# Performance work log

Measured on AMD Instinct MI355X. Metric: run time of the kernel, lower is better.

The kernel has to match this reference:

```python
import jax, jax.numpy as jnp
import numpy as np

L, B, N, C, H = 8, 8, 512, 1024, 16
D = C // H
TP = (2.0 * D) ** 0.5  # temperature_coeff * head_dim, sqrt


def _ln(x):
    # LayerNorm(eps=1e-6, no affine)
    m = jnp.mean(x, axis=-1, keepdims=True)
    v = jnp.var(x, axis=-1, keepdims=True)
    return (x - m) * jax.lax.rsqrt(v + 1e-6)


def _modulate(x, shift, scale):
    return x * (1 + scale) + shift


def setup_inputs() -> dict:
    key = jax.random.key(0)
    ks = jax.random.split(key, 18)
    s = 0.02
    return {
        "x": jax.random.normal(ks[0], (B, N, C), dtype=jnp.float32),
        "time": jax.random.uniform(ks[1], (B, 1), dtype=jnp.float32) * 100.0,
        "label": jax.random.normal(ks[2], (B, 2), dtype=jnp.float32),
        "x_mask": jax.random.randint(ks[3], (B, N, 1), 0, 2).astype(jnp.float32),
        # ValueLabelEmbed: Linear(2 -> C)
        "Wl": jax.random.normal(ks[4], (C, 2), dtype=jnp.float32) * s,
        "bl": jnp.zeros((C,), dtype=jnp.float32),
        # per-layer stacked weights (leading dim L)
        "Wq": jax.random.normal(ks[5], (L, C, C), dtype=jnp.float32) * s,
        "Wk": jax.random.normal(ks[6], (L, C, C), dtype=jnp.float32) * s,
        "Wv": jax.random.normal(ks[7], (L, C, C), dtype=jnp.float32) * s,
        "W1": jax.random.normal(ks[8], (L, 4 * C, C), dtype=jnp.float32) * s,
        "b1": jnp.zeros((L, 4 * C), dtype=jnp.float32),
        "W2": jax.random.normal(ks[9], (L, C, 4 * C), dtype=jnp.float32) * s,
        "b2": jnp.zeros((L, C), dtype=jnp.float32),
        "Wm": jax.random.normal(ks[10], (L, 6 * C, C), dtype=jnp.float32) * s,
        "bm": jnp.zeros((L, 6 * C), dtype=jnp.float32),
        # FinalLayer
        "Wf": jax.random.normal(ks[11], (C, C), dtype=jnp.float32) * s,
        "bf": jnp.zeros((C,), dtype=jnp.float32),
        "Wmf": jax.random.normal(ks[12], (2 * C, C), dtype=jnp.float32) * s,
        "bmf": jnp.zeros((2 * C,), dtype=jnp.float32),
    }


def reference(x, time, label, x_mask, Wl, bl, Wq, Wk, Wv, W1, b1, W2, b2, Wm, bm, Wf, bf, Wmf, bmf):
    # ValueLabelEmbed: (B,2) -> (B,1,C)
    lemb = (label @ Wl.T + bl)[:, None, :]
    # TimeEmbedding: interleaved sin/cos of time / 10000^(2i/d)
    base = jnp.power(10000.0, 2.0 * jnp.arange(C, dtype=jnp.float32) / C)
    te = time / base  # (B, C)
    even = (jnp.arange(C) % 2) == 0
    te = jnp.where(even, jnp.sin(te), jnp.cos(te))
    c = lemb + te[:, None, :]  # (B,1,C)

    # self-attention mask: True where exactly one of the pair is valid
    xm = x_mask[:, :, 0]  # (B,N)
    mask = ((xm[:, :, None] + xm[:, None, :]) == 1.0)[:, None, :, :]  # (B,1,N,N)

    def block(xc, p):
        wq, wk, wv, w1, bb1, w2, bb2, wm, bbm = p
        m6 = jax.nn.selu(c) @ wm.T + bbm  # (B,1,6C)
        sm, sc, gm, sf, cf, gf = jnp.split(m6, 6, axis=-1)
        h = _modulate(_ln(xc), sm, sc) * x_mask
        q = (h @ wq.T).reshape(B, N, H, D)
        k = (h @ wk.T).reshape(B, N, H, D)
        v = (h @ wv.T).reshape(B, N, H, D)
        scores = jnp.einsum('bqhd,bkhd->bhqk', q, k) / TP
        scores = jnp.where(mask, -jnp.inf, scores)
        alpha = jax.nn.softmax(scores, axis=-1)
        att = jnp.einsum('bhqk,bkhd->bqhd', alpha, v).reshape(B, N, C)
        xc = xc + gm * att
        h2 = _modulate(_ln(xc), sf, cf)
        ffn = jax.nn.selu(h2 @ w1.T + bb1) @ w2.T + bb2
        xc = (xc + gf * ffn) * x_mask
        return xc, None

    x, _ = jax.lax.scan(block, x, (Wq, Wk, Wv, W1, b1, W2, b2, Wm, bm))

    # FinalLayer
    m2 = jax.nn.selu(c) @ Wmf.T + bmf
    shift, scale = jnp.split(m2, 2, axis=-1)
    out = (_modulate(_ln(x), shift, scale) @ Wf.T + bf) * x_mask
    return out
```

## Files before the change

### kernel.cpp

```cpp
#include <hip/hip_runtime.h>
#include <hip/hip_bf16.h>
#include <cstddef>

#define DEVI __device__ __forceinline__

typedef __attribute__((ext_vector_type(4))) float f4v;
typedef __attribute__((ext_vector_type(16))) float f16v;
typedef __attribute__((ext_vector_type(8))) short s8v;
typedef __attribute__((ext_vector_type(4))) short s4v;

using bf16 = __hip_bfloat16;

constexpr float SELU_A = 1.6732632423543772f;
constexpr float SELU_S = 1.0507009873554805f;
constexpr float TPINV  = 0.08838834764831845f;

DEVI float bfbits(short s) { return __uint_as_float(((unsigned)(unsigned short)s) << 16); }
DEVI unsigned short f2bu(float f) {
  bf16 h = __float2bfloat16(f);
  return __builtin_bit_cast(unsigned short, h);
}
DEVI float seluf(float x) { return x > 0.f ? SELU_S * x : SELU_S * SELU_A * (__expf(x) - 1.f); }

DEVI void gl16(const void* g, void* l) {
  __builtin_amdgcn_global_load_lds((__attribute__((address_space(1))) void*)g,
                                   (__attribute__((address_space(3))) void*)l, 16, 0, 0);
}

DEVI void conv8(const float* __restrict__ src, bf16* __restrict__ dst) {
  f4v a = *(const f4v*)src;
  f4v b = *(const f4v*)(src + 4);
  s8v o;
  #pragma unroll
  for (int j = 0; j < 4; j++) { o[j] = (short)f2bu(a[j]); o[4 + j] = (short)f2bu(b[j]); }
  *(s8v*)dst = o;
}

__global__ void k_compact(const float* __restrict__ xm, int* __restrict__ idx,
                          int* __restrict__ pos, int* __restrict__ cnt,
                          int* __restrict__ start, int* __restrict__ t2b)
{
  int t = threadIdx.x;
  int b = t >> 6, lane = t & 63;
  __shared__ int scnt[8];
  int base = b * 512 + lane * 8;
  int mb[8]; int lc = 0;
  #pragma unroll
  for (int i = 0; i < 8; i++) { mb[i] = (xm[base + i] != 0.f) ? 1 : 0; lc += mb[i]; }
  int s = lc;
  #pragma unroll
  for (int o = 1; o < 64; o <<= 1) { int tt = __shfl_up(s, o); if (lane >= o) s += tt; }
  int run = s - lc;
  #pragma unroll
  for (int i = 0; i < 8; i++) {
    int n = lane * 8 + i;
    if (mb[i]) { idx[b * 512 + run] = n; pos[b * 512 + n] = run; run++; }
    else pos[b * 512 + n] = -1;
  }
  if (lane == 63) scnt[b] = s;
  __syncthreads();
  if (t == 0) {
    int st = 0, tile = 0;
    for (int bb = 0; bb < 8; bb++) {
      cnt[bb] = scnt[bb];
      start[bb] = st;
      int nt = (scnt[bb] + 127) >> 7;
      for (int k = 0; k < nt; k++) t2b[tile++] = bb;
      st += nt * 128;
    }
    start[8] = st;
    for (; tile < 32; tile++) t2b[tile] = 0;
  }
}

__global__ __launch_bounds__(256) void k_gather(const float* __restrict__ xin,
    const int* __restrict__ idx, const int* __restrict__ cnt,
    const int* __restrict__ start, const int* __restrict__ t2b,
    float* __restrict__ xc)
{
  int row = blockIdx.x, t = threadIdx.x;
  if (row >= start[8]) return;
  int tb = t2b[row >> 7], slot = row - start[tb];
  f4v v = {0.f, 0.f, 0.f, 0.f};
  if (slot < cnt[tb])
    v = *(const f4v*)&xin[((size_t)tb * 512 + idx[tb * 512 + slot]) * 1024 + t * 4];
  *(f4v*)&xc[(size_t)row * 1024 + t * 4] = v;
}

__global__ __launch_bounds__(256) void k_scatter(const float* __restrict__ ffin,
    const int* __restrict__ pos, const int* __restrict__ start, float* __restrict__ out)
{
  int row = blockIdx.x, t = threadIdx.x, b = row >> 9;
  int p = pos[row];
  f4v v = {0.f, 0.f, 0.f, 0.f};
  if (p >= 0) v = *(const f4v*)&ffin[(size_t)(start[b] + p) * 1024 + t * 4];
  *(f4v*)&out[(size_t)row * 1024 + t * 4] = v;
}

__global__ __launch_bounds__(256) void k_convall(
    const float* __restrict__ wq, const float* __restrict__ wk, const float* __restrict__ wv,
    const float* __restrict__ w1, const float* __restrict__ w2,
    bf16* __restrict__ wqkvb, bf16* __restrict__ w1b, bf16* __restrict__ w2b)
{
  int i = blockIdx.x * 256 + threadIdx.x;
  if (i < 393216) {
    int o = i * 8;
    int row = o >> 10, col = o & 1023;
    int sel = row >> 10, sr = row & 1023;
    conv8((sel == 0 ? wq : sel == 1 ? wk : wv) + (size_t)sr * 1024 + col, wqkvb + o);
  } else if (i < 917504) {
    size_t o = (size_t)(i - 393216) * 8;
    conv8(w1 + o, w1b + o);
  } else if (i < 1441792) {
    size_t o = (size_t)(i - 917504) * 8;
    conv8(w2 + o, w2b + o);
  }
}

__global__ void k_cond(const float* __restrict__ tim, const float* __restrict__ lab,
                       const float* __restrict__ Wl, const float* __restrict__ bl,
                       float* __restrict__ cs)
{
  int b = blockIdx.x, t = threadIdx.x;
  float l0 = lab[b * 2 + 0], l1 = lab[b * 2 + 1], tv = tim[b];
  #pragma unroll
  for (int i = 0; i < 4; i++) {
    int j = t + 256 * i;
    float e = powf(10000.f, (2.f * (float)j) * (1.f / 1024.f));
    float arg = tv / e;
    float te = ((j & 1) == 0) ? sinf(arg) : cosf(arg);
    float c = l0 * Wl[j * 2 + 0] + l1 * Wl[j * 2 + 1] + bl[j] + te;
    cs[b * 1024 + j] = seluf(c);
  }
}

__global__ __launch_bounds__(256) void k_small(
    const float* __restrict__ cs, const float* __restrict__ W, const float* __restrict__ bias,
    float* __restrict__ out, int O, int mode)
{
  __shared__ float cls[8192];
  int t = threadIdx.x;
  #pragma unroll
  for (int i = 0; i < 8; i++)
    *(f4v*)&cls[i * 1024 + t * 4] = *(const f4v*)&cs[i * 1024 + t * 4];
  __syncthreads();
  int w = t >> 6, l = t & 63;
  int o = blockIdx.x * 4 + w;
  if (o >= O) return;
  float acc[8] = {0.f, 0.f, 0.f, 0.f, 0.f, 0.f, 0.f, 0.f};
  const float* Wr = W + (size_t)o * 1024;
  for (int i = 0; i < 16; i++) {
    int k = i * 64 + l;
    float wv = Wr[k];
    #pragma unroll
    for (int b = 0; b < 8; b++) acc[b] += wv * cls[b * 1024 + k];
  }
  #pragma unroll
  for (int b = 0; b < 8; b++) {
    #pragma unroll
    for (int off = 32; off; off >>= 1) acc[b] += __shfl_xor(acc[b], off);
  }
  float bv = bias[o];
  #pragma unroll
  for (int b = 0; b < 8; b++) {
    if (l == b) {
      float val = acc[b] + bv;
      size_t dst;
      if (mode == 0) { int ll = o / 6144, ft = o - ll * 6144; dst = ((size_t)ll * 8 + b) * 6144 + ft; }
      else dst = (size_t)b * 2048 + o;
      out[dst] = val;
    }
  }
}

__global__ __launch_bounds__(256) void k_lnmod(
    const float* __restrict__ x, const float* __restrict__ shiftB, const float* __restrict__ scaleB,
    int bstride, const int* __restrict__ cnt, const int* __restrict__ start,
    const int* __restrict__ t2b, bf16* __restrict__ out)
{
  int row = blockIdx.x, t = threadIdx.x;
  if (row >= start[8]) return;
  int tb = t2b[row >> 7], slot = row - start[tb];
  if (slot >= cnt[tb]) {
    s4v z = {0, 0, 0, 0};
    *(s4v*)&out[(size_t)row * 1024 + t * 4] = z;
    return;
  }
  const float* xr = x + (size_t)row * 1024;
  f4v v = *(const f4v*)&xr[t * 4];
  float s = v[0] + v[1] + v[2] + v[3];
  float ss = v[0]*v[0] + v[1]*v[1] + v[2]*v[2] + v[3]*v[3];
  #pragma unroll
  for (int off = 32; off; off >>= 1) { s += __shfl_xor(s, off); ss += __shfl_xor(ss, off); }
  __shared__ float rs[4], rss[4];
  int w = t >> 6;
  if ((t & 63) == 0) { rs[w] = s; rss[w] = ss; }
  __syncthreads();
  s = rs[0] + rs[1] + rs[2] + rs[3];
  ss = rss[0] + rss[1] + rss[2] + rss[3];
  float mean = s * (1.f / 1024.f);
  float var = ss * (1.f / 1024.f) - mean * mean;
  float rstd = rsqrtf(var + 1e-6f);
  f4v sh = *(const f4v*)&shiftB[(size_t)tb * bstride + t * 4];
  f4v sc = *(const f4v*)&scaleB[(size_t)tb * bstride + t * 4];
  s4v o;
  #pragma unroll
  for (int i = 0; i < 4; i++)
    o[i] = (short)f2bu((v[i] - mean) * rstd * (1.f + sc[i]) + sh[i]);
  *(s4v*)&out[(size_t)row * 1024 + t * 4] = o;
}

__global__ __launch_bounds__(256) void k_resid(
    float* __restrict__ x, const bf16* __restrict__ att, const float* __restrict__ m6b,
    const int* __restrict__ cnt, const int* __restrict__ start,
    const int* __restrict__ t2b, bf16* __restrict__ h2)
{
  int row = blockIdx.x, t = threadIdx.x;
  if (row >= start[8]) return;
  int tb = t2b[row >> 7], slot = row - start[tb];
  if (slot >= cnt[tb]) {
    s4v z = {0, 0, 0, 0};
    *(s4v*)&h2[(size_t)row * 1024 + t * 4] = z;
    return;
  }
  float* xr = x + (size_t)row * 1024;
  const float* gm = m6b + (size_t)tb * 6144 + 2048;
  const float* sf = m6b + (size_t)tb * 6144 + 3072;
  const float* cf = m6b + (size_t)tb * 6144 + 4096;
  f4v xv = *(const f4v*)&xr[t * 4];
  s4v av = *(const s4v*)&att[((size_t)tb * 512 + slot) * 1024 + t * 4];
  f4v gv = *(const f4v*)&gm[t * 4];
  f4v vv;
  #pragma unroll
  for (int i = 0; i < 4; i++) vv[i] = xv[i] + gv[i] * bfbits(av[i]);
  *(f4v*)&xr[t * 4] = vv;
  float s = vv[0] + vv[1] + vv[2] + vv[3];
  float ss = vv[0]*vv[0] + vv[1]*vv[1] + vv[2]*vv[2] + vv[3]*vv[3];
  #pragma unroll
  for (int off = 32; off; off >>= 1) { s += __shfl_xor(s, off); ss += __shfl_xor(ss, off); }
  __shared__ float rs[4], rss[4];
  int w = t >> 6;
  if ((t & 63) == 0) { rs[w] = s; rss[w] = ss; }
  __syncthreads();
  s = rs[0] + rs[1] + rs[2] + rs[3];
  ss = rss[0] + rss[1] + rss[2] + rss[3];
  float mean = s * (1.f / 1024.f);
  float var = ss * (1.f / 1024.f) - mean * mean;
  float rstd = rsqrtf(var + 1e-6f);
  f4v sfv = *(const f4v*)&sf[t * 4];
  f4v cfv = *(const f4v*)&cf[t * 4];
  s4v o;
  #pragma unroll
  for (int i = 0; i < 4; i++)
    o[i] = (short)f2bu((vv[i] - mean) * rstd * (1.f + cfv[i]) + sfv[i]);
  *(s4v*)&h2[(size_t)row * 1024 + t * 4] = o;
}

__global__ __launch_bounds__(256) void k_attn(
    const bf16* __restrict__ q, const bf16* __restrict__ k, const bf16* __restrict__ vt,
    const int* __restrict__ cnt, bf16* __restrict__ att,
    const float* __restrict__ nwq, const float* __restrict__ nwk, const float* __restrict__ nwv,
    const float* __restrict__ nw1, const float* __restrict__ nw2,
    bf16* __restrict__ dqkv, bf16* __restrict__ dw1, bf16* __restrict__ dw2, int mode)
{
  if (blockIdx.x >= 4) {
    int cid = (blockIdx.x - 4) * 128 + blockIdx.y;
    int i0 = cid * 256 + threadIdx.x;
    #pragma unroll
    for (int half = 0; half < 2; half++) {
      int j = i0 * 2 + half;
      if (mode == 1) {
        if (j < 131072) conv8(nwq + (size_t)j * 8, dqkv + (size_t)j * 8);
      } else {
        if (j < 393216) {
          int o = j * 8;
          int row = o >> 10, col = o & 1023;
          int sel = row >> 10, sr = row & 1023;
          conv8((sel == 0 ? nwq : sel == 1 ? nwk : nwv) + (size_t)sr * 1024 + col, dqkv + o);
        } else if (j < 917504) {
          size_t o = (size_t)(j - 393216) * 8;
          conv8(nw1 + o, dw1 + o);
        } else {
          size_t o = (size_t)(j - 917504) * 8;
          conv8(nw2 + o, dw2 + o);
        }
      }
    }
    return;
  }

  int bh = blockIdx.y, b = bh >> 4, hh = bh & 15;
  int cntb = cnt[b];
  if ((int)blockIdx.x * 128 >= cntb) return;
  int t = threadIdx.x, w = t >> 6, lane = t & 63;
  int fr = lane & 15, g = lane >> 4;
  int qw = blockIdx.x * 128 + w * 32;
  const size_t ho = (size_t)bh * (512 * 64);

  __shared__ bf16 Pb[4][32][72];

  s8v qf[2][2];
  #pragma unroll
  for (int mf = 0; mf < 2; mf++)
    #pragma unroll
    for (int kk = 0; kk < 2; kk++)
      qf[mf][kk] = *(const s8v*)(q + ho + (size_t)(qw + mf * 16 + fr) * 64 + kk * 32 + g * 8);

  float mrow[2][4], lsum[2][4];
  f4v oacc[2][4];
  const f4v vzero = {0.f, 0.f, 0.f, 0.f};
  #pragma unroll
  for (int mf = 0; mf < 2; mf++)
    #pragma unroll
    for (int r = 0; r < 4; r++) { mrow[mf][r] = -3.0e38f; lsum[mf][r] = 0.f; }
  #pragma unroll
  for (int mf = 0; mf < 2; mf++)
    #pragma unroll
    for (int nd = 0; nd < 4; nd++) oacc[mf][nd] = vzero;

  int nkt = (cntb + 63) >> 6;
  for (int kt = 0; kt < nkt; kt++) {
    int kb0 = kt * 64;
    f4v sacc[2][4];
    #pragma unroll
    for (int mf = 0; mf < 2; mf++)
      #pragma unroll
      for (int nf = 0; nf < 4; nf++) sacc[mf][nf] = vzero;
    #pragma unroll
    for (int kk = 0; kk < 2; kk++) {
      s8v kf[4];
      #pragma unroll
      for (int nf = 0; nf < 4; nf++)
        kf[nf] = *(const s8v*)(k + ho + (size_t)(kb0 + nf * 16 + fr) * 64 + kk * 32 + g * 8);
      #pragma unroll
      for (int mf = 0; mf < 2; mf++)
        #pragma unroll
        for (int nf = 0; nf < 4; nf++)
          sacc[mf][nf] = __builtin_amdgcn_mfma_f32_16x16x32_bf16(qf[mf][kk], kf[nf], sacc[mf][nf], 0, 0, 0);
    }
    #pragma unroll
    for (int mf = 0; mf < 2; mf++) {
      #pragma unroll
      for (int r = 0; r < 4; r++) {
        float mx = -3.0e38f;
        #pragma unroll
        for (int nf = 0; nf < 4; nf++) {
          float s = sacc[mf][nf][r] * TPINV;
          if (kb0 + nf * 16 + fr >= cntb) s = -1.0e30f;
          sacc[mf][nf][r] = s;
          mx = fmaxf(mx, s);
        }
        mx = fmaxf(mx, __shfl_xor(mx, 1));
        mx = fmaxf(mx, __shfl_xor(mx, 2));
        mx = fmaxf(mx, __shfl_xor(mx, 4));
        mx = fmaxf(mx, __shfl_xor(mx, 8));
        float mnew = fmaxf(mrow[mf][r], mx);
        float corr = __expf(mrow[mf][r] - mnew);
        mrow[mf][r] = mnew;
        float ps = 0.f;
        #pragma unroll
        for (int nf = 0; nf < 4; nf++) {
          float p = __expf(sacc[mf][nf][r] - mnew);
          ps += p;
          Pb[w][mf * 16 + g * 4 + r][nf * 16 + fr] = __float2bfloat16(p);
        }
        lsum[mf][r] = lsum[mf][r] * corr + ps;
        #pragma unroll
        for (int nd = 0; nd < 4; nd++) oacc[mf][nd][r] *= corr;
      }
    }
    #pragma unroll
    for (int kk = 0; kk < 2; kk++) {
      s8v pf[2], vf[4];
      #pragma unroll
      for (int mf = 0; mf < 2; mf++)
        pf[mf] = *(const s8v*)&Pb[w][mf * 16 + fr][kk * 32 + g * 8];
      #pragma unroll
      for (int nd = 0; nd < 4; nd++)
        vf[nd] = *(const s8v*)(vt + ho + (size_t)(nd * 16 + fr) * 512 + kb0 + kk * 32 + g * 8);
      #pragma unroll
      for (int mf = 0; mf < 2; mf++)
        #pragma unroll
        for (int nd = 0; nd < 4; nd++)
          oacc[mf][nd] = __builtin_amdgcn_mfma_f32_16x16x32_bf16(pf[mf], vf[nd], oacc[mf][nd], 0, 0, 0);
    }
  }
  float inv[2][4];
  #pragma unroll
  for (int mf = 0; mf < 2; mf++)
    #pragma unroll
    for (int r = 0; r < 4; r++) {
      float ls = lsum[mf][r];
      ls += __shfl_xor(ls, 1);
      ls += __shfl_xor(ls, 2);
      ls += __shfl_xor(ls, 4);
      ls += __shfl_xor(ls, 8);
      inv[mf][r] = 1.f / ls;
    }
  #pragma unroll
  for (int mf = 0; mf < 2; mf++)
    #pragma unroll
    for (int nd = 0; nd < 4; nd++)
      #pragma unroll
      for (int r = 0; r < 4; r++) {
        int row = qw + mf * 16 + g * 4 + r;
        att[(size_t)(b * 512 + row) * 1024 + hh * 64 + nd * 16 + fr] =
            __float2bfloat16(oacc[mf][nd][r] * inv[mf][r]);
      }
}

template <int EPI, int BN>
__global__ __launch_bounds__(256) void k_gemm(
    const bf16* __restrict__ A, const bf16* __restrict__ W,
    const float* __restrict__ bias, int Kst, int kLen, int Ncols,
    const int* __restrict__ cnt, const int* __restrict__ start, const int* __restrict__ t2b,
    bf16* __restrict__ outb, float* __restrict__ outf)
{
  constexpr int NFR = BN / 64;
  constexpr int NW  = BN / 32;
  __shared__ bf16 As[128][64];
  __shared__ bf16 Ws[BN][64];
  int t = threadIdx.x, lane = t & 63, w = t >> 6;
  int wr = w >> 1, wc = w & 1;
  int m0 = blockIdx.y * 128, n0 = blockIdx.x * BN;
  if (m0 >= start[8]) return;
  int kOff = blockIdx.z * kLen;
  int r32 = lane & 31, hi = lane >> 5;

  const bf16* Abase = A + (size_t)m0 * Kst + kOff;
  const bf16* Wbase = W + (size_t)n0 * Kst + kOff;

  f16v acc[2][NFR];
  #pragma unroll
  for (int i = 0; i < 2; i++)
    #pragma unroll
    for (int j = 0; j < NFR; j++)
      #pragma unroll
      for (int e = 0; e < 16; e++) acc[i][j][e] = 0.f;

  int nkt = kLen >> 6;
  for (int kt = 0; kt < nkt; kt++) {
    int k0 = kt << 6;
    __syncthreads();
    #pragma unroll
    for (int i = 0; i < 4; i++) {
      int Z = w * 4096 + i * 1024 + lane * 16;
      int row = Z >> 7, slot = (Z >> 4) & 7;
      int ss = slot ^ (row & 7);
      gl16(Abase + (size_t)row * Kst + k0 + ss * 8, (char*)As + Z);
    }
    #pragma unroll
    for (int i = 0; i < NW; i++) {
      int Z = w * (NW * 1024) + i * 1024 + lane * 16;
      int row = Z >> 7, slot = (Z >> 4) & 7;
      int ss = slot ^ (row & 7);
      gl16(Wbase + (size_t)row * Kst + k0 + ss * 8, (char*)Ws + Z);
    }
    __syncthreads();
    #pragma unroll
    for (int kk = 0; kk < 4; kk++) {
      s8v af[2], bfr[NFR];
      #pragma unroll
      for (int mf = 0; mf < 2; mf++) {
        int row = wr * 64 + mf * 32 + r32;
        int sl = (kk * 2 + hi) ^ (row & 7);
        af[mf] = *(const s8v*)((const char*)As + row * 128 + sl * 16);
      }
      #pragma unroll
      for (int nf = 0; nf < NFR; nf++) {
        int row = wc * (BN / 2) + nf * 32 + r32;
        int sl = (kk * 2 + hi) ^ (row & 7);
        bfr[nf] = *(const s8v*)((const char*)Ws + row * 128 + sl * 16);
      }
      #pragma unroll
      for (int mf = 0; mf < 2; mf++)
        #pragma unroll
        for (int nf = 0; nf < NFR; nf++)
          acc[mf][nf] = __builtin_amdgcn_mfma_f32_32x32x16_bf16(af[mf], bfr[nf], acc[mf][nf], 0, 0, 0);
    }
  }

  int tb = t2b[m0 >> 7];
  int sb = start[tb];
  #pragma unroll
  for (int mf = 0; mf < 2; mf++) {
    #pragma unroll
    for (int nf = 0; nf < NFR; nf++) {
      int col = n0 + wc * (BN / 2) + nf * 32 + r32;
      #pragma unroll
      for (int qd = 0; qd < 4; qd++) {
        int row0 = m0 + wr * 64 + mf * 32 + qd * 8 + hi * 4;
        if (EPI == 0) {
          int sel = col >> 10, cl = col & 1023;
          int nn = row0 - sb;
          int h2 = cl >> 6, dd = cl & 63;
          if (sel == 2) {
            s4v o4;
            #pragma unroll
            for (int r = 0; r < 4; r++) o4[r] = (short)f2bu(acc[mf][nf][qd * 4 + r]);
            *(s4v*)&outb[(size_t)2 * 4194304 + (((size_t)tb * 16 + h2) * 64 + dd) * 512 + nn] = o4;
          } else {
            #pragma unroll
            for (int r = 0; r < 4; r++)
              outb[(size_t)sel * 4194304 + (((size_t)tb * 16 + h2) * 512 + (nn + r)) * 64 + dd] =
                  __float2bfloat16(acc[mf][nf][qd * 4 + r]);
          }
        } else {
          #pragma unroll
          for (int r = 0; r < 4; r++) {
            int row = row0 + r;
            float val = acc[mf][nf][qd * 4 + r];
            if (EPI == 1) {
              outb[(size_t)row * Ncols + col] = __float2bfloat16(seluf(val + bias[col]));
            } else if (EPI == 3) {
              outf[(size_t)row * 1024 + col] = val + bias[col];
            } else {
              outb[(size_t)blockIdx.z * 4194304 + (size_t)row * 1024 + col] = __float2bfloat16(val);
            }
          }
        }
      }
    }
  }
}

__global__ __launch_bounds__(256) void k_comb(
    const bf16* __restrict__ part, const float* __restrict__ bias,
    const float* __restrict__ gfb, const float* __restrict__ shiftN,
    const float* __restrict__ scaleN, int strideN,
    float* __restrict__ x, const int* __restrict__ cnt, const int* __restrict__ start,
    const int* __restrict__ t2b, bf16* __restrict__ h)
{
  int row = blockIdx.x, t = threadIdx.x;
  if (row >= start[8]) return;
  int tb = t2b[row >> 7], slot = row - start[tb];
  if (slot >= cnt[tb]) return;
  size_t o = (size_t)row * 1024 + t * 4;
  f4v sum = {0.f, 0.f, 0.f, 0.f};
  #pragma unroll
  for (int p = 0; p < 8; p++) {
    s4v pv = *(const s4v*)&part[o + (size_t)p * 4194304];
    #pragma unroll
    for (int i = 0; i < 4; i++) sum[i] += bfbits(pv[i]);
  }
  f4v bv = *(const f4v*)&bias[t * 4];
  f4v gf = *(const f4v*)&gfb[(size_t)tb * 6144 + t * 4];
  f4v xv = *(const f4v*)&x[o];
  f4v vv;
  #pragma unroll
  for (int i = 0; i < 4; i++)
    vv[i] = xv[i] + gf[i] * (sum[i] + bv[i]);
  *(f4v*)&x[o] = vv;
  float s = vv[0] + vv[1] + vv[2] + vv[3];
  float ss = vv[0]*vv[0] + vv[1]*vv[1] + vv[2]*vv[2] + vv[3]*vv[3];
  #pragma unroll
  for (int off = 32; off; off >>= 1) { s += __shfl_xor(s, off); ss += __shfl_xor(ss, off); }
  __shared__ float rs[4], rss[4];
  int w = t >> 6;
  if ((t & 63) == 0) { rs[w] = s; rss[w] = ss; }
  __syncthreads();
  s = rs[0] + rs[1] + rs[2] + rs[3];
  ss = rss[0] + rss[1] + rss[2] + rss[3];
  float mean = s * (1.f / 1024.f);
  float var = ss * (1.f / 1024.f) - mean * mean;
  float rstd = rsqrtf(var + 1e-6f);
  f4v sh = *(const f4v*)&shiftN[(size_t)tb * strideN + t * 4];
  f4v sc = *(const f4v*)&scaleN[(size_t)tb * strideN + t * 4];
  s4v ho;
  #pragma unroll
  for (int i = 0; i < 4; i++)
    ho[i] = (short)f2bu((vv[i] - mean) * rstd * (1.f + sc[i]) + sh[i]);
  *(s4v*)&h[(size_t)row * 1024 + t * 4] = ho;
}

extern "C" void kernel_launch(void* const* d_in, const int* in_sizes, int n_in,
                              void* d_out, int out_size, void* d_ws, size_t ws_size,
                              hipStream_t stream)
{
  const float* x_in  = (const float*)d_in[0];
  const float* tim   = (const float*)d_in[1];
  const float* lab   = (const float*)d_in[2];
  const float* xmask = (const float*)d_in[3];
  const float* Wl  = (const float*)d_in[4];
  const float* bl  = (const float*)d_in[5];
  const float* Wq  = (const float*)d_in[6];
  const float* Wk  = (const float*)d_in[7];
  const float* Wv  = (const float*)d_in[8];
  const float* W1  = (const float*)d_in[9];
  const float* b1  = (const float*)d_in[10];
  const float* W2  = (const float*)d_in[11];
  const float* b2  = (const float*)d_in[12];
  const float* Wm  = (const float*)d_in[13];
  const float* bm  = (const float*)d_in[14];
  const float* Wf  = (const float*)d_in[15];
  const float* bfp = (const float*)d_in[16];
  const float* Wmf = (const float*)d_in[17];
  const float* bmf = (const float*)d_in[18];

  char* ws = (char*)d_ws;
  float* x     = (float*)(ws + 0);
  float* cs    = (float*)(ws + 16777216);
  float* mAll  = (float*)(ws + 16809984);
  float* m2v   = (float*)(ws + 18382848);
  bf16*  h     = (bf16*)(ws + 18448384);
  bf16*  qb    = (bf16*)(ws + 26836992);
  bf16*  kb    = (bf16*)(ws + 35225600);
  bf16*  vb    = (bf16*)(ws + 43614208);
  bf16*  att   = (bf16*)(ws + 52002816);
  bf16*  f1    = (bf16*)(ws + 60391424);
  bf16*  wqkv0 = (bf16*)(ws + 93945856);
  bf16*  w1b0  = (bf16*)(ws + 100237312);
  bf16*  w2b0  = (bf16*)(ws + 108625920);
  bf16*  wfb   = (bf16*)(ws + 117014528);
  float* ffin  = (float*)(ws + 119111680);
  int*   idxb  = (int*)(ws + 135888896);
  int*   posb  = (int*)(ws + 135905280);
  int*   cntb  = (int*)(ws + 135921664);
  int*   strtb = (int*)(ws + 135921728);
  int*   t2bb  = (int*)(ws + 135921792);
  bf16*  wqkv1 = (bf16*)(ws + 135921920);
  bf16*  w1b1  = (bf16*)(ws + 142213376);
  bf16*  w2b1  = (bf16*)(ws + 150601984);
  bf16*  part  = (bf16*)(ws + 158990592);

  bf16* wqkvS[2] = { wqkv0, wqkv1 };
  bf16* w1S[2]   = { w1b0, w1b1 };
  bf16* w2S[2]   = { w2b0, w2b1 };

  k_compact<<<1, 512, 0, stream>>>(xmask, idxb, posb, cntb, strtb, t2bb);
  k_gather<<<4096, 256, 0, stream>>>(x_in, idxb, cntb, strtb, t2bb, x);

  k_cond<<<8, 256, 0, stream>>>(tim, lab, Wl, bl, cs);
  k_small<<<12288, 256, 0, stream>>>(cs, Wm, bm, mAll, 49152, 0);
  k_small<<<512, 256, 0, stream>>>(cs, Wmf, bmf, m2v, 2048, 1);

  k_convall<<<5632, 256, 0, stream>>>(Wq, Wk, Wv, W1, W2, wqkv0, w1b0, w2b0);
  k_lnmod<<<4096, 256, 0, stream>>>(x, mAll + 0, mAll + 1024, 6144, cntb, strtb, t2bb, h);

  for (int l = 0; l < 8; l++) {
    const float* m6b = mAll + (size_t)l * 49152;
    int sel = l & 1, nsel = sel ^ 1;
    int last = (l == 7);

    k_gemm<0, 64><<<dim3(48, 32), 256, 0, stream>>>(h, wqkvS[sel], nullptr, 1024, 1024, 3072,
                                                    cntb, strtb, t2bb, qb, nullptr);
    if (!last) {
      k_attn<<<dim3(26, 128), 256, 0, stream>>>(qb, kb, vb, cntb, att,
          Wq + (size_t)(l + 1) * 1048576, Wk + (size_t)(l + 1) * 1048576,
          Wv + (size_t)(l + 1) * 1048576, W1 + (size_t)(l + 1) * 4194304,
          W2 + (size_t)(l + 1) * 4194304,
          wqkvS[nsel], w1S[nsel], w2S[nsel], 0);
    } else {
      k_attn<<<dim3(26, 128), 256, 0, stream>>>(qb, kb, vb, cntb, att,
          Wf, Wf, Wf, Wf, Wf, wfb, wfb, wfb, 1);
    }
    k_resid<<<4096, 256, 0, stream>>>(x, att, m6b, cntb, strtb, t2bb, h);
    k_gemm<1, 64><<<dim3(64, 32), 256, 0, stream>>>(h, w1S[sel], b1 + l * 4096, 1024, 1024, 4096,
                                                    cntb, strtb, t2bb, f1, nullptr);
    k_gemm<4, 128><<<dim3(8, 32, 8), 256, 0, stream>>>(f1, w2S[sel], nullptr, 4096, 512, 1024,
                                                       cntb, strtb, t2bb, part, nullptr);
    const float* nShift = last ? m2v : (mAll + (size_t)(l + 1) * 49152);
    const float* nScale = last ? (m2v + 1024) : (mAll + (size_t)(l + 1) * 49152 + 1024);
    int nStride = last ? 2048 : 6144;
    k_comb<<<4096, 256, 0, stream>>>(part, b2 + l * 1024, m6b + 5120,
                                     nShift, nScale, nStride,
                                     x, cntb, strtb, t2bb, h);
  }

  k_gemm<3, 64><<<dim3(16, 32), 256, 0, stream>>>(h, wfb, bfp, 1024, 1024, 1024,
                                                  cntb, strtb, t2bb, nullptr, ffin);
  k_scatter<<<4096, 256, 0, stream>>>(ffin, posb, strtb, (float*)d_out);
}
```

Baseline: 1.366 ms.

## Halve GEMM M-tile to 64 rows and merge prologue kernels into one launch

```diff
diff --git a/kernel.cpp b/kernel.cpp
--- a/kernel.cpp
+++ b/kernel.cpp
@@ -65,26 +65,87 @@
       cnt[bb] = scnt[bb];
       start[bb] = st;
       int nt = (scnt[bb] + 127) >> 7;
-      for (int k = 0; k < nt; k++) t2b[tile++] = bb;
+      for (int k = 0; k < nt * 2; k++) t2b[tile++] = bb;
       st += nt * 128;
     }
     start[8] = st;
-    for (; tile < 32; tile++) t2b[tile] = 0;
-  }
-}
-
-__global__ __launch_bounds__(256) void k_gather(const float* __restrict__ xin,
-    const int* __restrict__ idx, const int* __restrict__ cnt,
-    const int* __restrict__ start, const int* __restrict__ t2b,
-    float* __restrict__ xc)
-{
-  int row = blockIdx.x, t = threadIdx.x;
-  if (row >= start[8]) return;
-  int tb = t2b[row >> 7], slot = row - start[tb];
-  f4v v = {0.f, 0.f, 0.f, 0.f};
-  if (slot < cnt[tb])
-    v = *(const f4v*)&xin[((size_t)tb * 512 + idx[tb * 512 + slot]) * 1024 + t * 4];
-  *(f4v*)&xc[(size_t)row * 1024 + t * 4] = v;
+    for (; tile < 64; tile++) t2b[tile] = 0;
+  }
+}
+
+__global__ __launch_bounds__(256) void k_prolog(
+    const float* __restrict__ xin, const int* __restrict__ idx, const int* __restrict__ cnt,
+    const int* __restrict__ start, const int* __restrict__ t2b, float* __restrict__ xc,
+    const float* __restrict__ wq, const float* __restrict__ wk, const float* __restrict__ wv,
+    const float* __restrict__ w1, const float* __restrict__ w2,
+    bf16* __restrict__ wqkvb, bf16* __restrict__ w1b, bf16* __restrict__ w2b,
+    const float* __restrict__ cs, const float* __restrict__ Wm, const float* __restrict__ bm,
+    float* __restrict__ mAll, const float* __restrict__ Wmf, const float* __restrict__ bmf,
+    float* __restrict__ m2v)
+{
+  int bid = blockIdx.x, t = threadIdx.x;
+  __shared__ float cls[8192];
+  if (bid < 4096) {
+    int row = bid;
+    if (row >= start[8]) return;
+    int tb = t2b[row >> 6], slot = row - start[tb];
+    f4v v = {0.f, 0.f, 0.f, 0.f};
+    if (slot < cnt[tb])
+      v = *(const f4v*)&xin[((size_t)tb * 512 + idx[tb * 512 + slot]) * 1024 + t * 4];
+    *(f4v*)&xc[(size_t)row * 1024 + t * 4] = v;
+  } else if (bid < 9728) {
+    int i = (bid - 4096) * 256 + t;
+    if (i < 393216) {
+      int o = i * 8;
+      int row = o >> 10, col = o & 1023;
+      int sel = row >> 10, sr = row & 1023;
+      conv8((sel == 0 ? wq : sel == 1 ? wk : wv) + (size_t)sr * 1024 + col, wqkvb + o);
+    } else if (i < 917504) {
+      size_t o = (size_t)(i - 393216) * 8;
+      conv8(w1 + o, w1b + o);
+    } else {
+      size_t o = (size_t)(i - 917504) * 8;
+      conv8(w2 + o, w2b + o);
+    }
+  } else {
+    int mode = (bid < 22016) ? 0 : 1;
+    const float* W = mode ? Wmf : Wm;
+    const float* bias = mode ? bmf : bm;
+    float* out = mode ? m2v : mAll;
+    int O = mode ? 2048 : 49152;
+    int ob = mode ? (bid - 22016) : (bid - 9728);
+    #pragma unroll
+    for (int i = 0; i < 8; i++)
+      *(f4v*)&cls[i * 1024 + t * 4] = *(const f4v*)&cs[i * 1024 + t * 4];
+    __syncthreads();
+    int w = t >> 6, l = t & 63;
+    int o = ob * 4 + w;
+    if (o >= O) return;
+    float acc[8] = {0.f, 0.f, 0.f, 0.f, 0.f, 0.f, 0.f, 0.f};
+    const float* Wr = W + (size_t)o * 1024;
+    for (int i = 0; i < 16; i++) {
+      int k = i * 64 + l;
+      float wv2 = Wr[k];
+      #pragma unroll
+      for (int b = 0; b < 8; b++) acc[b] += wv2 * cls[b * 1024 + k];
+    }
+    #pragma unroll
+    for (int b = 0; b < 8; b++) {
+      #pragma unroll
+      for (int off = 32; off; off >>= 1) acc[b] += __shfl_xor(acc[b], off);
+    }
+    float bv = bias[o];
+    #pragma unroll
+    for (int b = 0; b < 8; b++) {
+      if (l == b) {
+        float val = acc[b] + bv;
+        size_t dst;
+        if (mode == 0) { int ll = o / 6144, ft = o - ll * 6144; dst = ((size_t)ll * 8 + b) * 6144 + ft; }
+        else dst = (size_t)b * 2048 + o;
+        out[dst] = val;
+      }
+    }
+  }
 }
 
 __global__ __launch_bounds__(256) void k_scatter(const float* __restrict__ ffin,
@@ -95,26 +156,6 @@
   f4v v = {0.f, 0.f, 0.f, 0.f};
   if (p >= 0) v = *(const f4v*)&ffin[(size_t)(start[b] + p) * 1024 + t * 4];
   *(f4v*)&out[(size_t)row * 1024 + t * 4] = v;
-}
-
-__global__ __launch_bounds__(256) void k_convall(
-    const float* __restrict__ wq, const float* __restrict__ wk, const float* __restrict__ wv,
-    const float* __restrict__ w1, const float* __restrict__ w2,
-    bf16* __restrict__ wqkvb, bf16* __restrict__ w1b, bf16* __restrict__ w2b)
-{
-  int i = blockIdx.x * 256 + threadIdx.x;
-  if (i < 393216) {
-    int o = i * 8;
-    int row = o >> 10, col = o & 1023;
-    int sel = row >> 10, sr = row & 1023;
-    conv8((sel == 0 ? wq : sel == 1 ? wk : wv) + (size_t)sr * 1024 + col, wqkvb + o);
-  } else if (i < 917504) {
-    size_t o = (size_t)(i - 393216) * 8;
-    conv8(w1 + o, w1b + o);
-  } else if (i < 1441792) {
-    size_t o = (size_t)(i - 917504) * 8;
-    conv8(w2 + o, w2b + o);
-  }
 }
 
 __global__ void k_cond(const float* __restrict__ tim, const float* __restrict__ lab,
@@ -134,45 +175,6 @@
   }
 }
 
-__global__ __launch_bounds__(256) void k_small(
-    const float* __restrict__ cs, const float* __restrict__ W, const float* __restrict__ bias,
-    float* __restrict__ out, int O, int mode)
-{
-  __shared__ float cls[8192];
-  int t = threadIdx.x;
-  #pragma unroll
-  for (int i = 0; i < 8; i++)
-    *(f4v*)&cls[i * 1024 + t * 4] = *(const f4v*)&cs[i * 1024 + t * 4];
-  __syncthreads();
-  int w = t >> 6, l = t & 63;
-  int o = blockIdx.x * 4 + w;
-  if (o >= O) return;
-  float acc[8] = {0.f, 0.f, 0.f, 0.f, 0.f, 0.f, 0.f, 0.f};
-  const float* Wr = W + (size_t)o * 1024;
-  for (int i = 0; i < 16; i++) {
-    int k = i * 64 + l;
-    float wv = Wr[k];
-    #pragma unroll
-    for (int b = 0; b < 8; b++) acc[b] += wv * cls[b * 1024 + k];
-  }
-  #pragma unroll
-  for (int b = 0; b < 8; b++) {
-    #pragma unroll
-    for (int off = 32; off; off >>= 1) acc[b] += __shfl_xor(acc[b], off);
-  }
-  float bv = bias[o];
-  #pragma unroll
-  for (int b = 0; b < 8; b++) {
-    if (l == b) {
-      float val = acc[b] + bv;
-      size_t dst;
-      if (mode == 0) { int ll = o / 6144, ft = o - ll * 6144; dst = ((size_t)ll * 8 + b) * 6144 + ft; }
-      else dst = (size_t)b * 2048 + o;
-      out[dst] = val;
-    }
-  }
-}
-
 __global__ __launch_bounds__(256) void k_lnmod(
     const float* __restrict__ x, const float* __restrict__ shiftB, const float* __restrict__ scaleB,
     int bstride, const int* __restrict__ cnt, const int* __restrict__ start,
@@ -180,7 +182,7 @@
 {
   int row = blockIdx.x, t = threadIdx.x;
   if (row >= start[8]) return;
-  int tb = t2b[row >> 7], slot = row - start[tb];
+  int tb = t2b[row >> 6], slot = row - start[tb];
   if (slot >= cnt[tb]) {
     s4v z = {0, 0, 0, 0};
     *(s4v*)&out[(size_t)row * 1024 + t * 4] = z;
@@ -217,7 +219,7 @@
 {
   int row = blockIdx.x, t = threadIdx.x;
   if (row >= start[8]) return;
-  int tb = t2b[row >> 7], slot = row - start[tb];
+  int tb = t2b[row >> 6], slot = row - start[tb];
   if (slot >= cnt[tb]) {
     s4v z = {0, 0, 0, 0};
     *(s4v*)&h2[(size_t)row * 1024 + t * 4] = z;
@@ -409,20 +411,22 @@
       }
 }
 
-template <int EPI, int BN>
+template <int EPI, int BM, int BN>
 __global__ __launch_bounds__(256) void k_gemm(
     const bf16* __restrict__ A, const bf16* __restrict__ W,
     const float* __restrict__ bias, int Kst, int kLen, int Ncols,
     const int* __restrict__ cnt, const int* __restrict__ start, const int* __restrict__ t2b,
     bf16* __restrict__ outb, float* __restrict__ outf)
 {
+  constexpr int MFR = BM / 64;
   constexpr int NFR = BN / 64;
+  constexpr int NA  = BM / 32;
   constexpr int NW  = BN / 32;
-  __shared__ bf16 As[128][64];
+  __shared__ bf16 As[BM][64];
   __shared__ bf16 Ws[BN][64];
   int t = threadIdx.x, lane = t & 63, w = t >> 6;
   int wr = w >> 1, wc = w & 1;
-  int m0 = blockIdx.y * 128, n0 = blockIdx.x * BN;
+  int m0 = blockIdx.y * BM, n0 = blockIdx.x * BN;
   if (m0 >= start[8]) return;
   int kOff = blockIdx.z * kLen;
   int r32 = lane & 31, hi = lane >> 5;
@@ -430,9 +434,9 @@
   const bf16* Abase = A + (size_t)m0 * Kst + kOff;
   const bf16* Wbase = W + (size_t)n0 * Kst + kOff;
 
-  f16v acc[2][NFR];
-  #pragma unroll
-  for (int i = 0; i < 2; i++)
+  f16v acc[MFR][NFR];
+  #pragma unroll
+  for (int i = 0; i < MFR; i++)
     #pragma unroll
     for (int j = 0; j < NFR; j++)
       #pragma unroll
@@ -443,8 +447,8 @@
     int k0 = kt << 6;
     __syncthreads();
     #pragma unroll
-    for (int i = 0; i < 4; i++) {
-      int Z = w * 4096 + i * 1024 + lane * 16;
+    for (int i = 0; i < NA; i++) {
+      int Z = w * (NA * 1024) + i * 1024 + lane * 16;
       int row = Z >> 7, slot = (Z >> 4) & 7;
       int ss = slot ^ (row & 7);
       gl16(Abase + (size_t)row * Kst + k0 + ss * 8, (char*)As + Z);
@@ -459,10 +463,10 @@
     __syncthreads();
     #pragma unroll
     for (int kk = 0; kk < 4; kk++) {
-      s8v af[2], bfr[NFR];
-      #pragma unroll
-      for (int mf = 0; mf < 2; mf++) {
-        int row = wr * 64 + mf * 32 + r32;
+      s8v af[MFR], bfr[NFR];
+      #pragma unroll
+      for (int mf = 0; mf < MFR; mf++) {
+        int row = wr * (BM / 2) + mf * 32 + r32;
         int sl = (kk * 2 + hi) ^ (row & 7);
         af[mf] = *(const s8v*)((const char*)As + row * 128 + sl * 16);
       }
@@ -473,23 +477,23 @@
         bfr[nf] = *(const s8v*)((const char*)Ws + row * 128 + sl * 16);
       }
       #pragma unroll
-      for (int mf = 0; mf < 2; mf++)
+      for (int mf = 0; mf < MFR; mf++)
         #pragma unroll
         for (int nf = 0; nf < NFR; nf++)
           acc[mf][nf] = __builtin_amdgcn_mfma_f32_32x32x16_bf16(af[mf], bfr[nf], acc[mf][nf], 0, 0, 0);
     }
   }
 
-  int tb = t2b[m0 >> 7];
+  int tb = t2b[m0 >> 6];
   int sb = start[tb];
   #pragma unroll
-  for (int mf = 0; mf < 2; mf++) {
+  for (int mf = 0; mf < MFR; mf++) {
     #pragma unroll
     for (int nf = 0; nf < NFR; nf++) {
       int col = n0 + wc * (BN / 2) + nf * 32 + r32;
       #pragma unroll
       for (int qd = 0; qd < 4; qd++) {
-        int row0 = m0 + wr * 64 + mf * 32 + qd * 8 + hi * 4;
+        int row0 = m0 + wr * (BM / 2) + mf * 32 + qd * 8 + hi * 4;
         if (EPI == 0) {
           int sel = col >> 10, cl = col & 1023;
           int nn = row0 - sb;
@@ -533,7 +537,7 @@
 {
   int row = blockIdx.x, t = threadIdx.x;
   if (row >= start[8]) return;
-  int tb = t2b[row >> 7], slot = row - start[tb];
+  int tb = t2b[row >> 6], slot = row - start[tb];
   if (slot >= cnt[tb]) return;
   size_t o = (size_t)row * 1024 + t * 4;
   f4v sum = {0.f, 0.f, 0.f, 0.f};
@@ -618,23 +622,20 @@
   int*   cntb  = (int*)(ws + 135921664);
   int*   strtb = (int*)(ws + 135921728);
   int*   t2bb  = (int*)(ws + 135921792);
-  bf16*  wqkv1 = (bf16*)(ws + 135921920);
-  bf16*  w1b1  = (bf16*)(ws + 142213376);
-  bf16*  w2b1  = (bf16*)(ws + 150601984);
-  bf16*  part  = (bf16*)(ws + 158990592);
+  bf16*  wqkv1 = (bf16*)(ws + 135925760);
+  bf16*  w1b1  = (bf16*)(ws + 142217216);
+  bf16*  w2b1  = (bf16*)(ws + 150605824);
+  bf16*  part  = (bf16*)(ws + 158994432);
 
   bf16* wqkvS[2] = { wqkv0, wqkv1 };
   bf16* w1S[2]   = { w1b0, w1b1 };
   bf16* w2S[2]   = { w2b0, w2b1 };
 
   k_compact<<<1, 512, 0, stream>>>(xmask, idxb, posb, cntb, strtb, t2bb);
-  k_gather<<<4096, 256, 0, stream>>>(x_in, idxb, cntb, strtb, t2bb, x);
-
   k_cond<<<8, 256, 0, stream>>>(tim, lab, Wl, bl, cs);
-  k_small<<<12288, 256, 0, stream>>>(cs, Wm, bm, mAll, 49152, 0);
-  k_small<<<512, 256, 0, stream>>>(cs, Wmf, bmf, m2v, 2048, 1);
-
-  k_convall<<<5632, 256, 0, stream>>>(Wq, Wk, Wv, W1, W2, wqkv0, w1b0, w2b0);
+  k_prolog<<<22528, 256, 0, stream>>>(x_in, idxb, cntb, strtb, t2bb, x,
+                                      Wq, Wk, Wv, W1, W2, wqkv0, w1b0, w2b0,
+                                      cs, Wm, bm, mAll, Wmf, bmf, m2v);
   k_lnmod<<<4096, 256, 0, stream>>>(x, mAll + 0, mAll + 1024, 6144, cntb, strtb, t2bb, h);
 
   for (int l = 0; l < 8; l++) {
@@ -642,8 +643,8 @@
     int sel = l & 1, nsel = sel ^ 1;
     int last = (l == 7);
 
-    k_gemm<0, 64><<<dim3(48, 32), 256, 0, stream>>>(h, wqkvS[sel], nullptr, 1024, 1024, 3072,
-                                                    cntb, strtb, t2bb, qb, nullptr);
+    k_gemm<0, 64, 64><<<dim3(48, 64), 256, 0, stream>>>(h, wqkvS[sel], nullptr, 1024, 1024, 3072,
+                                                        cntb, strtb, t2bb, qb, nullptr);
     if (!last) {
       k_attn<<<dim3(26, 128), 256, 0, stream>>>(qb, kb, vb, cntb, att,
           Wq + (size_t)(l + 1) * 1048576, Wk + (size_t)(l + 1) * 1048576,
@@ -655,10 +656,10 @@
           Wf, Wf, Wf, Wf, Wf, wfb, wfb, wfb, 1);
     }
     k_resid<<<4096, 256, 0, stream>>>(x, att, m6b, cntb, strtb, t2bb, h);
-    k_gemm<1, 64><<<dim3(64, 32), 256, 0, stream>>>(h, w1S[sel], b1 + l * 4096, 1024, 1024, 4096,
-                                                    cntb, strtb, t2bb, f1, nullptr);
-    k_gemm<4, 128><<<dim3(8, 32, 8), 256, 0, stream>>>(f1, w2S[sel], nullptr, 4096, 512, 1024,
-                                                       cntb, strtb, t2bb, part, nullptr);
+    k_gemm<1, 64, 64><<<dim3(64, 64), 256, 0, stream>>>(h, w1S[sel], b1 + l * 4096, 1024, 1024, 4096,
+                                                        cntb, strtb, t2bb, f1, nullptr);
+    k_gemm<4, 128, 128><<<dim3(8, 32, 8), 256, 0, stream>>>(f1, w2S[sel], nullptr, 4096, 512, 1024,
+                                                            cntb, strtb, t2bb, part, nullptr);
     const float* nShift = last ? m2v : (mAll + (size_t)(l + 1) * 49152);
     const float* nScale = last ? (m2v + 1024) : (mAll + (size_t)(l + 1) * 49152 + 1024);
     int nStride = last ? 2048 : 6144;
@@ -667,7 +668,7 @@
                                      x, cntb, strtb, t2bb, h);
   }
 
-  k_gemm<3, 64><<<dim3(16, 32), 256, 0, stream>>>(h, wfb, bfp, 1024, 1024, 1024,
-                                                  cntb, strtb, t2bb, nullptr, ffin);
+  k_gemm<3, 64, 64><<<dim3(16, 64), 256, 0, stream>>>(h, wfb, bfp, 1024, 1024, 1024,
+                                                      cntb, strtb, t2bb, nullptr, ffin);
   k_scatter<<<4096, 256, 0, stream>>>(ffin, posb, strtb, (float*)d_out);
 }
```

Result: slower. 1.424 ms (+4.2%).
